# Optimization experiments

Measured on AMD Instinct MI355X. Metric: run time of the kernel, lower is better.

Reference implementation:

```python
import jax, jax.numpy as jnp
import numpy as np

N, E, H, IN, ED = 10000, 160000, 8, 128, 32
C1, C2 = 128, 128  # per-head channels of conv1 and conv2_1


def gat_conv(x, edge_index, edge_attr, W, We, att_s, att_d, att_e, bias, concat):
    """PyG GATConv with edge_dim, add_self_loops=True (fill_value='mean'), eval mode."""
    n = x.shape[0]
    h, c = att_s.shape
    src, dst = edge_index[0], edge_index[1]
    # self-loop edge_attr = per-node mean of incoming edge attrs (PyG fill_value='mean')
    deg = jax.ops.segment_sum(jnp.ones((src.shape[0],), x.dtype), dst, num_segments=n)
    loop_attr = jax.ops.segment_sum(edge_attr, dst, num_segments=n) / jnp.maximum(deg, 1.0)[:, None]
    loop = jnp.arange(n)
    src = jnp.concatenate([src, loop])
    dst = jnp.concatenate([dst, loop])
    ea = jnp.concatenate([edge_attr, loop_attr], axis=0)  # [E+N, ED]

    xh = (x @ W).reshape(n, h, c)                  # [N,H,C]
    a_s = jnp.sum(xh * att_s, axis=-1)             # [N,H]
    a_d = jnp.sum(xh * att_d, axis=-1)             # [N,H]
    eh = (ea @ We).reshape(-1, h, c)               # [E+N,H,C]
    a_e = jnp.sum(eh * att_e, axis=-1)             # [E+N,H]

    alpha = jax.nn.leaky_relu(a_s[src] + a_d[dst] + a_e, negative_slope=0.2)
    # segment softmax over incoming edges of each dst node (every node has a self loop)
    amax = jax.ops.segment_max(alpha, dst, num_segments=n)
    ex = jnp.exp(alpha - amax[dst])
    denom = jax.ops.segment_sum(ex, dst, num_segments=n)
    alpha = ex / (denom[dst] + 1e-16)

    out = jax.ops.segment_sum(xh[src] * alpha[:, :, None], dst, num_segments=n)  # [N,H,C]
    out = out.reshape(n, h * c) if concat else out.mean(axis=1)
    return out + bias


def setup_inputs() -> dict:
    key = jax.random.key(0)
    ks = jax.random.split(key, 16)
    s = 0.05
    return {
        "x": jax.random.normal(ks[0], (N, IN), jnp.float32),
        "edge_index": jax.random.randint(ks[1], (2, E), 0, N, dtype=jnp.int64),
        "edge_attr": jax.random.normal(ks[2], (E, ED), jnp.float32),
        # conv1: IN -> H*C1, concat=True
        "W1": jax.random.normal(ks[3], (IN, H * C1), jnp.float32) * s,
        "We1": jax.random.normal(ks[4], (ED, H * C1), jnp.float32) * s,
        "as1": jax.random.normal(ks[5], (H, C1), jnp.float32) * s,
        "ad1": jax.random.normal(ks[6], (H, C1), jnp.float32) * s,
        "ae1": jax.random.normal(ks[7], (H, C1), jnp.float32) * s,
        "b1": jnp.zeros((H * C1,), jnp.float32),
        # conv2_1: H*C1 -> C2, concat=False (Drugbank branch)
        "W2": jax.random.normal(ks[8], (H * C1, H * C2), jnp.float32) * s,
        "We2": jax.random.normal(ks[9], (ED, H * C2), jnp.float32) * s,
        "as2": jax.random.normal(ks[10], (H, C2), jnp.float32) * s,
        "ad2": jax.random.normal(ks[11], (H, C2), jnp.float32) * s,
        "ae2": jax.random.normal(ks[12], (H, C2), jnp.float32) * s,
        "b2": jnp.zeros((C2,), jnp.float32),
    }


def reference(x, edge_index, edge_attr, W1, We1, as1, ad1, ae1, b1,
              W2, We2, as2, ad2, ae2, b2):
    # dataset == 'Drugbank' path; dropout is identity in eval mode
    h = gat_conv(x, edge_index, edge_attr, W1, We1, as1, ad1, ae1, b1, concat=True)
    h = jax.nn.relu(h)
    out = gat_conv(h, edge_index, edge_attr, W2, We2, as2, ad2, ae2, b2, concat=False)
    return out
```

## Files before the change

kernel.cpp:

```cpp
#include <hip/hip_runtime.h>
#include <hip/hip_bf16.h>
#include <cstdint>
#include <cstddef>


#define EDD 32

typedef __attribute__((ext_vector_type(4))) float f32x4;
typedef __attribute__((ext_vector_type(8))) short bf16x8;
typedef __attribute__((ext_vector_type(8))) unsigned short u16x8;

__device__ inline unsigned short f2bf_rn(float f) {
  uint32_t u = __float_as_uint(f);
  return (unsigned short)((u + 0x7FFFu + ((u >> 16) & 1u)) >> 16);
}

__device__ inline float bf2f(unsigned short b) {
  return __uint_as_float(((uint32_t)b) << 16);
}

__device__ inline void gload_lds16(const void* g, void* l) {
  __builtin_amdgcn_global_load_lds((const __attribute__((address_space(1))) void*)g,
                                   (__attribute__((address_space(3))) void*)l, 16, 0, 0);
}


__global__ void deg_count_kernel(const int* __restrict__ ei, int* __restrict__ deg, int E) {
  int e = blockIdx.x * 256 + threadIdx.x;
  if (e < E) atomicAdd(&deg[ei[E + e]], 1);
}

__global__ void scan_kernel(const int* __restrict__ deg, int* __restrict__ rowptr,
                            int* __restrict__ cursor, int n) {
  __shared__ int wsum[16];
  int t = threadIdx.x;
  int chunk = (n + 1023) >> 10;
  int lo = min(t * chunk, n), hi = min(lo + chunk, n);
  int s = 0;
  for (int i = lo; i < hi; ++i) s += deg[i];
  int lane = t & 63, w = t >> 6;
  int v = s;
#pragma unroll
  for (int off = 1; off < 64; off <<= 1) {
    int u = __shfl_up(v, off);
    if (lane >= off) v += u;
  }
  if (lane == 63) wsum[w] = v;
  __syncthreads();
  if (t == 0) {
    int acc = 0;
#pragma unroll
    for (int i = 0; i < 16; ++i) { int x = wsum[i]; wsum[i] = acc; acc += x; }
  }
  __syncthreads();
  int excl = v - s + wsum[w];
  for (int i = lo; i < hi; ++i) {
    rowptr[i] = excl; cursor[i] = excl; excl += deg[i];
  }
  if (t == 1023) rowptr[n] = excl;
}

__global__ void scatter_kernel(const int* __restrict__ ei, int* __restrict__ cursor,
                               int* __restrict__ csr_src, int* __restrict__ csr_dst,
                               int* __restrict__ csr_eid, int E) {
  int e = blockIdx.x * 256 + threadIdx.x;
  if (e >= E) return;
  int d = ei[E + e];
  int pos = atomicAdd(&cursor[d], 1);
  csr_src[pos] = ei[e];
  csr_dst[pos] = d;
  csr_eid[pos] = e;
}

__global__ void permute_ea_kernel(const int* __restrict__ csr_eid,
                                  const float* __restrict__ edge_attr,
                                  float* __restrict__ ea_csr, int E) {
  int gid = blockIdx.x * 256 + threadIdx.x;
  if (gid >= E * 8) return;
  int p = gid >> 3, q = gid & 7;
  int e = csr_eid[p];
  ((float4*)ea_csr)[(size_t)p * 8 + q] = ((const float4*)edge_attr)[(size_t)e * 8 + q];
}

__global__ void loop_attr_kernel(const int* __restrict__ rowptr,
                                 const float* __restrict__ ea_csr,
                                 float* __restrict__ loop_attr, int N) {
  int n = blockIdx.x * 8 + (threadIdx.x >> 5);
  int lane = threadIdx.x & 31;
  if (n >= N) return;
  int r0 = rowptr[n], r1 = rowptr[n + 1];
  float s = 0.f;
  for (int p = r0; p < r1; ++p)
    s += ea_csr[(size_t)p * EDD + lane];
  float dv = fmaxf((float)(r1 - r0), 1.f);
  loop_attr[(size_t)n * EDD + lane] = s / dv;
}


__global__ void cvt_bf16_kernel(const float* __restrict__ in,
                                unsigned short* __restrict__ out, int n4) {
  int i = blockIdx.x * 256 + threadIdx.x;
  if (i >= n4) return;
  float4 v = ((const float4*)in)[i];
  ushort4 o;
  o.x = f2bf_rn(v.x); o.y = f2bf_rn(v.y); o.z = f2bf_rn(v.z); o.w = f2bf_rn(v.w);
  ((ushort4*)out)[i] = o;
}

__global__ void transpose_both_kernel(const float* __restrict__ W1, unsigned short* __restrict__ Bt1,
                                      const float* __restrict__ W2, unsigned short* __restrict__ Bt2) {
  __shared__ float tile[32][33];
  int by = blockIdx.y;
  const float* W; unsigned short* Bt; int K, bk;
  if (by < 4) { W = W1; Bt = Bt1; K = 128; bk = by * 32; }
  else        { W = W2; Bt = Bt2; K = 1024; bk = (by - 4) * 32; }
  int bn = blockIdx.x * 32;
  int tx = threadIdx.x & 31, ty = threadIdx.x >> 5;
  for (int r = ty; r < 32; r += 8)
    tile[r][tx] = W[(size_t)(bk + r) * 1024 + bn + tx];
  __syncthreads();
  for (int r = ty; r < 32; r += 8)
    Bt[(size_t)(bn + r) * K + bk + tx] = f2bf_rn(tile[tx][r]);
}

__global__ void ve_both_kernel(const float* __restrict__ We1, const float* __restrict__ ae1,
                               const float* __restrict__ We2, const float* __restrict__ ae2,
                               float* __restrict__ Ve) {
  int b = blockIdx.x;
  const float* We = b ? We2 : We1;
  const float* ae = b ? ae2 : ae1;
  int t = threadIdx.x;
  int d = t >> 3, h = t & 7;
  float s = 0.f;
  for (int c = 0; c < 128; ++c) s = fmaf(We[d * 1024 + h * 128 + c], ae[h * 128 + c], s);
  Ve[b * 256 + t] = s;
}


__global__ __launch_bounds__(256) void gemm1_fullk_kernel(
    const unsigned short* __restrict__ Abf, const unsigned short* __restrict__ Btbf,
    unsigned short* __restrict__ Cbf, float* __restrict__ a_s, float* __restrict__ a_d,
    const float* __restrict__ att_s, const float* __restrict__ att_d, int M) {
  __shared__ __align__(16) unsigned short lds[4 * 8192];
  __shared__ float redS[128][2];
  __shared__ float redD[128][2];
  const int t = threadIdx.x;
  const int lane = t & 63;
  const int wid = t >> 6;
  const int wr = wid >> 1, wc = wid & 1;
  const int m0 = blockIdx.y * 128;
  const int n0 = blockIdx.x * 128;
  const int hb = blockIdx.x;
  const int srow = lane >> 2;
  const int sg = lane & 3;

#pragma unroll
  for (int s = 0; s < 4; ++s) {
    unsigned short* L = lds + s * 8192;
    int k0 = s * 32;
#pragma unroll
    for (int q = 0; q < 2; ++q) {
      int rb = wid * 32 + q * 16;
      int row = rb + srow;
      int gsrc = sg ^ ((row >> 1) & 3);
      size_t ga = (size_t)(m0 + row) * 128 + k0 + gsrc * 8;
      size_t gb = (size_t)(n0 + row) * 128 + k0 + gsrc * 8;
      gload_lds16(Abf + ga, L + rb * 32);
      gload_lds16(Btbf + gb, L + 4096 + rb * 32);
    }
  }
  __syncthreads();

  int offa[4], offb[4];
#pragma unroll
  for (int i = 0; i < 4; ++i) {
    int rowa = wr * 64 + i * 16 + (lane & 15);
    offa[i] = rowa * 32 + (((lane >> 4) ^ ((rowa >> 1) & 3)) * 8);
    int rowb = wc * 64 + i * 16 + (lane & 15);
    offb[i] = rowb * 32 + (((lane >> 4) ^ ((rowb >> 1) & 3)) * 8);
  }

  f32x4 acc[4][4] = {};
#pragma unroll
  for (int s = 0; s < 4; ++s) {
    unsigned short* L = lds + s * 8192;
    bf16x8 ah[4];
#pragma unroll
    for (int i = 0; i < 4; ++i) ah[i] = *(const bf16x8*)(L + offa[i]);
#pragma unroll
    for (int j = 0; j < 4; ++j) {
      bf16x8 bh = *(const bf16x8*)(L + 4096 + offb[j]);
#pragma unroll
      for (int i = 0; i < 4; ++i)
        acc[i][j] = __builtin_amdgcn_mfma_f32_16x16x32_bf16(ah[i], bh, acc[i][j], 0, 0, 0);
    }
  }

  float as_v[4], ad_v[4];
#pragma unroll
  for (int j = 0; j < 4; ++j) {
    int c = n0 + wc * 64 + j * 16 + (lane & 15);
    as_v[j] = att_s[c];
    ad_v[j] = att_d[c];
  }
#pragma unroll
  for (int i = 0; i < 4; ++i) {
#pragma unroll
    for (int r = 0; r < 4; ++r) {
      float sA = 0.f, sD = 0.f;
#pragma unroll
      for (int j = 0; j < 4; ++j) {
        sA = fmaf(acc[i][j][r], as_v[j], sA);
        sD = fmaf(acc[i][j][r], ad_v[j], sD);
      }
#pragma unroll
      for (int mask = 1; mask <= 8; mask <<= 1) {
        sA += __shfl_xor(sA, mask);
        sD += __shfl_xor(sD, mask);
      }
      if ((lane & 15) == 0) {
        int ml = wr * 64 + i * 16 + (lane >> 4) * 4 + r;
        redS[ml][wc] = sA;
        redD[ml][wc] = sD;
      }
      int m = m0 + wr * 64 + i * 16 + (lane >> 4) * 4 + r;
      if (m < M) {
#pragma unroll
        for (int j = 0; j < 4; ++j) {
          int n = n0 + wc * 64 + j * 16 + (lane & 15);
          Cbf[(size_t)m * 1024 + n] = f2bf_rn(acc[i][j][r]);
        }
      }
    }
  }
  __syncthreads();
  if (t < 128) {
    int m = m0 + t;
    if (m < M) {
      a_s[(size_t)m * 8 + hb] = redS[t][0] + redS[t][1];
      a_d[(size_t)m * 8 + hb] = redD[t][0] + redD[t][1];
    }
  }
}


__global__ __launch_bounds__(256) void gemm2_dbuf_kernel(
    const unsigned short* __restrict__ Abf, const unsigned short* __restrict__ Btbf,
    unsigned short* __restrict__ Cbf, float* __restrict__ a_s, float* __restrict__ a_d,
    const float* __restrict__ att_s, const float* __restrict__ att_d, int M, int K) {
  __shared__ __align__(16) unsigned short lds[2 * 8192];
  __shared__ float redS[128][2];
  __shared__ float redD[128][2];
  const int t = threadIdx.x;
  const int lane = t & 63;
  const int wid = t >> 6;
  const int wr = wid >> 1, wc = wid & 1;
  const int m0 = blockIdx.y * 128;
  const int n0 = blockIdx.x * 128;
  const int hb = blockIdx.x;
  const int srow = lane >> 2;
  const int sg = lane & 3;
  const int nk = K >> 5;

  auto stage = [&](int b, int k) {
    unsigned short* L = lds + b * 8192;
    int k0 = k * 32;
#pragma unroll
    for (int q = 0; q < 2; ++q) {
      int rb = wid * 32 + q * 16;
      int row = rb + srow;
      int gsrc = sg ^ ((row >> 1) & 3);
      size_t ga = (size_t)(m0 + row) * K + k0 + gsrc * 8;
      size_t gb = (size_t)(n0 + row) * K + k0 + gsrc * 8;
      gload_lds16(Abf + ga, L + rb * 32);
      gload_lds16(Btbf + gb, L + 4096 + rb * 32);
    }
  };

  int offa[4], offb[4];
#pragma unroll
  for (int i = 0; i < 4; ++i) {
    int rowa = wr * 64 + i * 16 + (lane & 15);
    offa[i] = rowa * 32 + (((lane >> 4) ^ ((rowa >> 1) & 3)) * 8);
    int rowb = wc * 64 + i * 16 + (lane & 15);
    offb[i] = rowb * 32 + (((lane >> 4) ^ ((rowb >> 1) & 3)) * 8);
  }

  f32x4 acc[4][4] = {};
  stage(0, 0);
  __syncthreads();

  for (int k = 0; k < nk; ++k) {
    if (k + 1 < nk) stage((k + 1) & 1, k + 1);
    unsigned short* L = lds + (k & 1) * 8192;
    bf16x8 ah[4], bh[4];
#pragma unroll
    for (int i = 0; i < 4; ++i) ah[i] = *(const bf16x8*)(L + offa[i]);
#pragma unroll
    for (int j = 0; j < 4; ++j) bh[j] = *(const bf16x8*)(L + 4096 + offb[j]);
#pragma unroll
    for (int j = 0; j < 4; ++j)
#pragma unroll
      for (int i = 0; i < 4; ++i)
        acc[i][j] = __builtin_amdgcn_mfma_f32_16x16x32_bf16(ah[i], bh[j], acc[i][j], 0, 0, 0);
    __syncthreads();
  }

  float as_v[4], ad_v[4];
#pragma unroll
  for (int j = 0; j < 4; ++j) {
    int c = n0 + wc * 64 + j * 16 + (lane & 15);
    as_v[j] = att_s[c];
    ad_v[j] = att_d[c];
  }
#pragma unroll
  for (int i = 0; i < 4; ++i) {
#pragma unroll
    for (int r = 0; r < 4; ++r) {
      float sA = 0.f, sD = 0.f;
#pragma unroll
      for (int j = 0; j < 4; ++j) {
        sA = fmaf(acc[i][j][r], as_v[j], sA);
        sD = fmaf(acc[i][j][r], ad_v[j], sD);
      }
#pragma unroll
      for (int mask = 1; mask <= 8; mask <<= 1) {
        sA += __shfl_xor(sA, mask);
        sD += __shfl_xor(sD, mask);
      }
      if ((lane & 15) == 0) {
        int ml = wr * 64 + i * 16 + (lane >> 4) * 4 + r;
        redS[ml][wc] = sA;
        redD[ml][wc] = sD;
      }
      int m = m0 + wr * 64 + i * 16 + (lane >> 4) * 4 + r;
      if (m < M) {
#pragma unroll
        for (int j = 0; j < 4; ++j) {
          int n = n0 + wc * 64 + j * 16 + (lane & 15);
          Cbf[(size_t)m * 1024 + n] = f2bf_rn(acc[i][j][r]);
        }
      }
    }
  }
  __syncthreads();
  if (t < 128) {
    int m = m0 + t;
    if (m < M) {
      a_s[(size_t)m * 8 + hb] = redS[t][0] + redS[t][1];
      a_d[(size_t)m * 8 + hb] = redD[t][0] + redD[t][1];
    }
  }
}


__global__ __launch_bounds__(256) void edge_alpha_t_kernel(
    const int* __restrict__ csr_src, const int* __restrict__ csr_dst,
    const float* __restrict__ ea_csr, const float* __restrict__ loop_attr,
    const float* __restrict__ a_s, const float* __restrict__ a_d,
    const float* __restrict__ Ve,
    float* __restrict__ alpha_t, float* __restrict__ self_t, int E, int n) {
  __shared__ float sVe[EDD][8];
  int t = threadIdx.x;
  sVe[t >> 3][t & 7] = Ve[t];
  __syncthreads();
  int idx = blockIdx.x * 256 + t;
  if (idx >= E + n) return;
  int s, d;
  const float* ea;
  if (idx < E) {
    s = csr_src[idx]; d = csr_dst[idx];
    ea = ea_csr + (size_t)idx * EDD;
  } else {
    s = d = idx - E;
    ea = loop_attr + (size_t)(idx - E) * EDD;
  }
  float ae[8] = {0.f, 0.f, 0.f, 0.f, 0.f, 0.f, 0.f, 0.f};
#pragma unroll
  for (int k = 0; k < EDD; k += 4) {
    float4 v = *(const float4*)&ea[k];
#pragma unroll
    for (int h = 0; h < 8; ++h) {
      ae[h] = fmaf(v.x, sVe[k][h], ae[h]);
      ae[h] = fmaf(v.y, sVe[k + 1][h], ae[h]);
      ae[h] = fmaf(v.z, sVe[k + 2][h], ae[h]);
      ae[h] = fmaf(v.w, sVe[k + 3][h], ae[h]);
    }
  }
#pragma unroll
  for (int h = 0; h < 8; ++h) {
    float a = a_s[(size_t)s * 8 + h] + a_d[(size_t)d * 8 + h] + ae[h];
    a = (a > 0.f) ? a : 0.2f * a;
    if (idx < E) alpha_t[(size_t)h * E + idx] = a;
    else         self_t[(size_t)h * n + (idx - E)] = a;
  }
}


__global__ __launch_bounds__(256) void sm_weights_t_kernel(
    float* __restrict__ alpha_t, float* __restrict__ self_t,
    const int* __restrict__ rowptr, int N, int E) {
  int n = blockIdx.x * 4 + (threadIdx.x >> 6);
  int lane = threadIdx.x & 63;
  if (n >= N) return;
  int r0 = rowptr[n], deg = rowptr[n + 1] - r0;
  int h = lane >> 3, slot = lane & 7;
  float* pa = alpha_t + (size_t)h * E + r0;
  float m = -1e30f, s = 0.f;
  for (int i = slot; i < deg; i += 8) {
    float a = pa[i];
    if (a <= m) {
      s += __expf(a - m);
    } else {
      s = s * __expf(m - a) + 1.f;
      m = a;
    }
  }
#pragma unroll
  for (int mask = 1; mask <= 4; mask <<= 1) {
    float mo = __shfl_xor(m, mask);
    float so = __shfl_xor(s, mask);
    float mn = fmaxf(m, mo);
    s = s * __expf(m - mn) + so * __expf(mo - mn);
    m = mn;
  }
  float aself = self_t[(size_t)h * N + n];
  float mn = fmaxf(m, aself);
  s = s * __expf(m - mn) + __expf(aself - mn);
  float inv = 1.f / (s + 1e-16f);
  if (slot == 0) self_t[(size_t)h * N + n] = __expf(aself - mn) * inv;
  for (int i = slot; i < deg; i += 8)
    pa[i] = __expf(pa[i] - mn) * inv;
}


template <int RELU_BIAS>
__global__ __launch_bounds__(256) void agg_gather_h_kernel(
    const unsigned short* __restrict__ xbf, const float* __restrict__ alpha_t,
    const float* __restrict__ self_t, const int* __restrict__ rowptr,
    const int* __restrict__ csr_src, const float* __restrict__ bias,
    unsigned short* __restrict__ obf, int N, int E) {
  const int h = blockIdx.x & 7;
  const int g = blockIdx.x >> 3;
  const int t = threadIdx.x;
  const int n = g * 16 + (t >> 4);
  const int sub = t & 15;
  if (n >= N) return;
  const int r0 = rowptr[n], r1 = rowptr[n + 1];
  const float* __restrict__ pw = alpha_t + (size_t)h * E;
  const size_t cb = (size_t)h * 128 + sub * 8;
  float acc[8];
  {
    float ws = self_t[(size_t)h * N + n];
    u16x8 v = *(const u16x8*)(xbf + (size_t)n * 1024 + cb);
#pragma unroll
    for (int k = 0; k < 8; ++k) acc[k] = ws * bf2f(v[k]);
  }
  int p = r0;
  for (; p + 2 <= r1; p += 2) {
    float w0 = pw[p], w1 = pw[p + 1];
    int s0 = csr_src[p], s1 = csr_src[p + 1];
    u16x8 v0 = *(const u16x8*)(xbf + (size_t)s0 * 1024 + cb);
    u16x8 v1 = *(const u16x8*)(xbf + (size_t)s1 * 1024 + cb);
#pragma unroll
    for (int k = 0; k < 8; ++k) acc[k] = fmaf(w0, bf2f(v0[k]), acc[k]);
#pragma unroll
    for (int k = 0; k < 8; ++k) acc[k] = fmaf(w1, bf2f(v1[k]), acc[k]);
  }
  if (p < r1) {
    float w0 = pw[p];
    int s0 = csr_src[p];
    u16x8 v0 = *(const u16x8*)(xbf + (size_t)s0 * 1024 + cb);
#pragma unroll
    for (int k = 0; k < 8; ++k) acc[k] = fmaf(w0, bf2f(v0[k]), acc[k]);
  }
  u16x8 o;
  if (RELU_BIAS) {
    float4 b0 = *(const float4*)(bias + cb);
    float4 b1v = *(const float4*)(bias + cb + 4);
    float bb[8] = {b0.x, b0.y, b0.z, b0.w, b1v.x, b1v.y, b1v.z, b1v.w};
#pragma unroll
    for (int k = 0; k < 8; ++k) o[k] = f2bf_rn(fmaxf(acc[k] + bb[k], 0.f));
  } else {
#pragma unroll
    for (int k = 0; k < 8; ++k) o[k] = f2bf_rn(acc[k]);
  }
  *(u16x8*)(obf + (size_t)n * 1024 + cb) = o;
}


__global__ void head_reduce_kernel(const unsigned short* __restrict__ xpart,
                                   const float* __restrict__ b2,
                                   float* __restrict__ outp, int N) {
  int gid = blockIdx.x * 256 + threadIdx.x;
  if (gid >= N * 32) return;
  int n = gid >> 5, q = gid & 31;
  float sx = 0.f, sy = 0.f, sz = 0.f, sw = 0.f;
#pragma unroll
  for (int h = 0; h < 8; ++h) {
    ushort4 v = *(const ushort4*)(xpart + (size_t)n * 1024 + h * 128 + q * 4);
    sx += bf2f(v.x); sy += bf2f(v.y); sz += bf2f(v.z); sw += bf2f(v.w);
  }
  float4 b = ((const float4*)b2)[q];
  float4 o;
  o.x = sx * 0.125f + b.x;
  o.y = sy * 0.125f + b.y;
  o.z = sz * 0.125f + b.z;
  o.w = sw * 0.125f + b.w;
  ((float4*)outp)[(size_t)n * 32 + q] = o;
}


extern "C" void kernel_launch(void* const* d_in, const int* in_sizes, int n_in,
                              void* d_out, int out_size, void* d_ws, size_t ws_size,
                              hipStream_t stream) {
  const float* x        = (const float*)d_in[0];
  const int*   ei       = (const int*)d_in[1];
  const float* edge_attr= (const float*)d_in[2];
  const float* W1       = (const float*)d_in[3];
  const float* We1      = (const float*)d_in[4];
  const float* as1      = (const float*)d_in[5];
  const float* ad1      = (const float*)d_in[6];
  const float* ae1      = (const float*)d_in[7];
  const float* b1       = (const float*)d_in[8];
  const float* W2       = (const float*)d_in[9];
  const float* We2      = (const float*)d_in[10];
  const float* as2      = (const float*)d_in[11];
  const float* ad2      = (const float*)d_in[12];
  const float* ae2      = (const float*)d_in[13];
  const float* b2       = (const float*)d_in[14];
  float* out = (float*)d_out;

  const int N = in_sizes[0] / 128;
  const int E = in_sizes[2] / EDD;
  const int Mpad = ((N + 127) / 128) * 128;

  char* ws = (char*)d_ws;
  size_t off = 0;
  auto alloc = [&](size_t bytes) -> void* {
    void* p = ws + off;
    off = (off + bytes + 255) & ~(size_t)255;
    return p;
  };
  int*   deg       = (int*)alloc((size_t)N * 4);
  int*   rowptr    = (int*)alloc((size_t)(N + 1) * 4);
  int*   cursor    = (int*)alloc((size_t)N * 4);
  int*   csr_src   = (int*)alloc((size_t)E * 4);
  int*   csr_dst   = (int*)alloc((size_t)E * 4);
  int*   csr_eid   = (int*)alloc((size_t)E * 4);
  float* ea_csr    = (float*)alloc((size_t)E * EDD * 4);
  float* loop_attr = (float*)alloc((size_t)N * EDD * 4);
  float* a_s       = (float*)alloc((size_t)N * 8 * 4);
  float* a_d       = (float*)alloc((size_t)N * 8 * 4);
  float* Ve        = (float*)alloc(512 * 4);
  float* alpha_t   = (float*)alloc((size_t)E * 8 * 4);
  float* self_t    = (float*)alloc((size_t)N * 8 * 4);
  unsigned short* xh1bf = (unsigned short*)alloc((size_t)N * 1024 * 2);
  unsigned short* xh2bf = (unsigned short*)alloc((size_t)N * 1024 * 2);
  unsigned short* xpart = (unsigned short*)alloc((size_t)N * 1024 * 2);
  unsigned short* xbf   = (unsigned short*)alloc((size_t)Mpad * 128 * 2);
  unsigned short* Bt1   = (unsigned short*)alloc((size_t)1024 * 128 * 2);
  unsigned short* Bt2   = (unsigned short*)alloc((size_t)1024 * 1024 * 2);
  unsigned short* h1bf  = (unsigned short*)alloc((size_t)Mpad * 1024 * 2);
  (void)ws_size; (void)n_in; (void)out_size;

  hipMemsetAsync(deg, 0, (size_t)N * 4, stream);

  int gE = (E + 255) / 256;
  deg_count_kernel<<<gE, 256, 0, stream>>>(ei, deg, E);
  scan_kernel<<<1, 1024, 0, stream>>>(deg, rowptr, cursor, N);
  scatter_kernel<<<gE, 256, 0, stream>>>(ei, cursor, csr_src, csr_dst, csr_eid, E);
  permute_ea_kernel<<<(E * 8 + 255) / 256, 256, 0, stream>>>(csr_eid, edge_attr, ea_csr, E);
  loop_attr_kernel<<<(N + 7) / 8, 256, 0, stream>>>(rowptr, ea_csr, loop_attr, N);

  cvt_bf16_kernel<<<(N * 128 / 4 + 255) / 256, 256, 0, stream>>>(x, xbf, N * 128 / 4);
  transpose_both_kernel<<<dim3(32, 36), 256, 0, stream>>>(W1, Bt1, W2, Bt2);
  ve_both_kernel<<<2, 256, 0, stream>>>(We1, ae1, We2, ae2, Ve);

  dim3 ggrid(8, Mpad / 128);
  int gEA = (E + N + 255) / 256;
  int gSM = (N + 3) / 4;
  int gAG = 8 * ((N + 15) / 16);

  gemm1_fullk_kernel<<<ggrid, 256, 0, stream>>>(xbf, Bt1, xh1bf, a_s, a_d, as1, ad1, N);
  edge_alpha_t_kernel<<<gEA, 256, 0, stream>>>(csr_src, csr_dst, ea_csr, loop_attr,
                                               a_s, a_d, Ve, alpha_t, self_t, E, N);
  sm_weights_t_kernel<<<gSM, 256, 0, stream>>>(alpha_t, self_t, rowptr, N, E);
  agg_gather_h_kernel<1><<<gAG, 256, 0, stream>>>(xh1bf, alpha_t, self_t, rowptr, csr_src,
                                                  b1, h1bf, N, E);

  gemm2_dbuf_kernel<<<ggrid, 256, 0, stream>>>(h1bf, Bt2, xh2bf, a_s, a_d, as2, ad2, N, 1024);
  edge_alpha_t_kernel<<<gEA, 256, 0, stream>>>(csr_src, csr_dst, ea_csr, loop_attr,
                                               a_s, a_d, Ve + 256, alpha_t, self_t, E, N);
  sm_weights_t_kernel<<<gSM, 256, 0, stream>>>(alpha_t, self_t, rowptr, N, E);
  agg_gather_h_kernel<0><<<gAG, 256, 0, stream>>>(xh2bf, alpha_t, self_t, rowptr, csr_src,
                                                  nullptr, xpart, N, E);
  head_reduce_kernel<<<(N * 32 + 255) / 256, 256, 0, stream>>>(xpart, b2, out, N);
}
```

Before: 248.0 us.

## Fuse edge alpha with segment softmax, derive self-loop attr inline, register-load B

The separate per-edge alpha kernel and softmax kernel are merged into one per-node kernel. It computes edge logits, tracks an online max/sum, and gets the self-loop logit from the mean of edge logits, which holds because that logit is linear in edge_attr. This removes the loop_attr kernel, the csr_dst array and one round trip of alpha through memory. Separately, the second GEMM now loads B fragments straight from global memory into registers with prefetch, which halves LDS use but adds uncoalesced global loads and register pressure.

```diff
diff --git a/kernel.cpp b/kernel.cpp
--- a/kernel.cpp
+++ b/kernel.cpp
@@ -61,14 +61,12 @@
 }
 
 __global__ void scatter_kernel(const int* __restrict__ ei, int* __restrict__ cursor,
-                               int* __restrict__ csr_src, int* __restrict__ csr_dst,
-                               int* __restrict__ csr_eid, int E) {
+                               int* __restrict__ csr_src, int* __restrict__ csr_eid, int E) {
   int e = blockIdx.x * 256 + threadIdx.x;
   if (e >= E) return;
   int d = ei[E + e];
   int pos = atomicAdd(&cursor[d], 1);
   csr_src[pos] = ei[e];
-  csr_dst[pos] = d;
   csr_eid[pos] = e;
 }
 
@@ -80,20 +78,6 @@
   int p = gid >> 3, q = gid & 7;
   int e = csr_eid[p];
   ((float4*)ea_csr)[(size_t)p * 8 + q] = ((const float4*)edge_attr)[(size_t)e * 8 + q];
-}
-
-__global__ void loop_attr_kernel(const int* __restrict__ rowptr,
-                                 const float* __restrict__ ea_csr,
-                                 float* __restrict__ loop_attr, int N) {
-  int n = blockIdx.x * 8 + (threadIdx.x >> 5);
-  int lane = threadIdx.x & 31;
-  if (n >= N) return;
-  int r0 = rowptr[n], r1 = rowptr[n + 1];
-  float s = 0.f;
-  for (int p = r0; p < r1; ++p)
-    s += ea_csr[(size_t)p * EDD + lane];
-  float dv = fmaxf((float)(r1 - r0), 1.f);
-  loop_attr[(size_t)n * EDD + lane] = s / dv;
 }
 
 
@@ -244,11 +228,11 @@
 }
 
 
-__global__ __launch_bounds__(256) void gemm2_dbuf_kernel(
+__global__ __launch_bounds__(256) void gemm2_breg_kernel(
     const unsigned short* __restrict__ Abf, const unsigned short* __restrict__ Btbf,
     unsigned short* __restrict__ Cbf, float* __restrict__ a_s, float* __restrict__ a_d,
     const float* __restrict__ att_s, const float* __restrict__ att_d, int M, int K) {
-  __shared__ __align__(16) unsigned short lds[2 * 8192];
+  __shared__ __align__(16) unsigned short lds[2 * 4096];
   __shared__ float redS[128][2];
   __shared__ float redD[128][2];
   const int t = threadIdx.x;
@@ -262,8 +246,8 @@
   const int sg = lane & 3;
   const int nk = K >> 5;
 
-  auto stage = [&](int b, int k) {
-    unsigned short* L = lds + b * 8192;
+  auto stageA = [&](int b, int k) {
+    unsigned short* L = lds + b * 4096;
     int k0 = k * 32;
 #pragma unroll
     for (int q = 0; q < 2; ++q) {
@@ -271,38 +255,48 @@
       int row = rb + srow;
       int gsrc = sg ^ ((row >> 1) & 3);
       size_t ga = (size_t)(m0 + row) * K + k0 + gsrc * 8;
-      size_t gb = (size_t)(n0 + row) * K + k0 + gsrc * 8;
       gload_lds16(Abf + ga, L + rb * 32);
-      gload_lds16(Btbf + gb, L + 4096 + rb * 32);
     }
   };
 
-  int offa[4], offb[4];
+  const unsigned short* bbase = Btbf + (size_t)(n0 + wc * 64 + (lane & 15)) * K + (lane >> 4) * 8;
+  auto loadB = [&](bf16x8* b, int k0) {
+#pragma unroll
+    for (int j = 0; j < 4; ++j)
+      b[j] = *(const bf16x8*)(bbase + (size_t)j * 16 * K + k0);
+  };
+
+  int offa[4];
 #pragma unroll
   for (int i = 0; i < 4; ++i) {
     int rowa = wr * 64 + i * 16 + (lane & 15);
     offa[i] = rowa * 32 + (((lane >> 4) ^ ((rowa >> 1) & 3)) * 8);
-    int rowb = wc * 64 + i * 16 + (lane & 15);
-    offb[i] = rowb * 32 + (((lane >> 4) ^ ((rowb >> 1) & 3)) * 8);
   }
 
   f32x4 acc[4][4] = {};
-  stage(0, 0);
+  bf16x8 bcur[4], bnext[4];
+  stageA(0, 0);
+  loadB(bcur, 0);
   __syncthreads();
 
   for (int k = 0; k < nk; ++k) {
-    if (k + 1 < nk) stage((k + 1) & 1, k + 1);
-    unsigned short* L = lds + (k & 1) * 8192;
-    bf16x8 ah[4], bh[4];
+    if (k + 1 < nk) {
+      stageA((k + 1) & 1, k + 1);
+      loadB(bnext, (k + 1) * 32);
+    }
+    unsigned short* L = lds + (k & 1) * 4096;
+    bf16x8 ah[4];
 #pragma unroll
     for (int i = 0; i < 4; ++i) ah[i] = *(const bf16x8*)(L + offa[i]);
 #pragma unroll
-    for (int j = 0; j < 4; ++j) bh[j] = *(const bf16x8*)(L + 4096 + offb[j]);
-#pragma unroll
     for (int j = 0; j < 4; ++j)
 #pragma unroll
       for (int i = 0; i < 4; ++i)
-        acc[i][j] = __builtin_amdgcn_mfma_f32_16x16x32_bf16(ah[i], bh[j], acc[i][j], 0, 0, 0);
+        acc[i][j] = __builtin_amdgcn_mfma_f32_16x16x32_bf16(ah[i], bcur[j], acc[i][j], 0, 0, 0);
+    if (k + 1 < nk) {
+#pragma unroll
+      for (int j = 0; j < 4; ++j) bcur[j] = bnext[j];
+    }
     __syncthreads();
   }
 
@@ -354,61 +348,40 @@
 }
 
 
-__global__ __launch_bounds__(256) void edge_alpha_t_kernel(
-    const int* __restrict__ csr_src, const int* __restrict__ csr_dst,
-    const float* __restrict__ ea_csr, const float* __restrict__ loop_attr,
+__global__ __launch_bounds__(256) void alpha_sm_kernel(
+    const int* __restrict__ rowptr, const int* __restrict__ csr_src,
+    const float* __restrict__ ea_csr,
     const float* __restrict__ a_s, const float* __restrict__ a_d,
     const float* __restrict__ Ve,
-    float* __restrict__ alpha_t, float* __restrict__ self_t, int E, int n) {
+    float* __restrict__ alpha_t, float* __restrict__ self_t, int N, int E) {
   __shared__ float sVe[EDD][8];
   int t = threadIdx.x;
   sVe[t >> 3][t & 7] = Ve[t];
   __syncthreads();
-  int idx = blockIdx.x * 256 + t;
-  if (idx >= E + n) return;
-  int s, d;
-  const float* ea;
-  if (idx < E) {
-    s = csr_src[idx]; d = csr_dst[idx];
-    ea = ea_csr + (size_t)idx * EDD;
-  } else {
-    s = d = idx - E;
-    ea = loop_attr + (size_t)(idx - E) * EDD;
-  }
-  float ae[8] = {0.f, 0.f, 0.f, 0.f, 0.f, 0.f, 0.f, 0.f};
-#pragma unroll
-  for (int k = 0; k < EDD; k += 4) {
-    float4 v = *(const float4*)&ea[k];
-#pragma unroll
-    for (int h = 0; h < 8; ++h) {
-      ae[h] = fmaf(v.x, sVe[k][h], ae[h]);
-      ae[h] = fmaf(v.y, sVe[k + 1][h], ae[h]);
-      ae[h] = fmaf(v.z, sVe[k + 2][h], ae[h]);
-      ae[h] = fmaf(v.w, sVe[k + 3][h], ae[h]);
-    }
-  }
-#pragma unroll
-  for (int h = 0; h < 8; ++h) {
-    float a = a_s[(size_t)s * 8 + h] + a_d[(size_t)d * 8 + h] + ae[h];
+  int n = blockIdx.x * 4 + (t >> 6);
+  if (n >= N) return;
+  int lane = t & 63;
+  int e8 = lane >> 3, h = lane & 7;
+  int r0 = rowptr[n], deg = rowptr[n + 1] - r0;
+  float adn = a_d[(size_t)n * 8 + h];
+  float m = -1e30f, s = 0.f, aesum = 0.f;
+  for (int i = e8; i < deg; i += 8) {
+    int p = r0 + i;
+    int src = csr_src[p];
+    const float4* ea4 = (const float4*)(ea_csr + (size_t)p * EDD);
+    float ae = 0.f;
+#pragma unroll
+    for (int k = 0; k < 8; ++k) {
+      float4 v = ea4[k];
+      ae = fmaf(v.x, sVe[k * 4 + 0][h], ae);
+      ae = fmaf(v.y, sVe[k * 4 + 1][h], ae);
+      ae = fmaf(v.z, sVe[k * 4 + 2][h], ae);
+      ae = fmaf(v.w, sVe[k * 4 + 3][h], ae);
+    }
+    aesum += ae;
+    float a = a_s[(size_t)src * 8 + h] + adn + ae;
     a = (a > 0.f) ? a : 0.2f * a;
-    if (idx < E) alpha_t[(size_t)h * E + idx] = a;
-    else         self_t[(size_t)h * n + (idx - E)] = a;
-  }
-}
-
-
-__global__ __launch_bounds__(256) void sm_weights_t_kernel(
-    float* __restrict__ alpha_t, float* __restrict__ self_t,
-    const int* __restrict__ rowptr, int N, int E) {
-  int n = blockIdx.x * 4 + (threadIdx.x >> 6);
-  int lane = threadIdx.x & 63;
-  if (n >= N) return;
-  int r0 = rowptr[n], deg = rowptr[n + 1] - r0;
-  int h = lane >> 3, slot = lane & 7;
-  float* pa = alpha_t + (size_t)h * E + r0;
-  float m = -1e30f, s = 0.f;
-  for (int i = slot; i < deg; i += 8) {
-    float a = pa[i];
+    alpha_t[(size_t)h * E + p] = a;
     if (a <= m) {
       s += __expf(a - m);
     } else {
@@ -417,20 +390,25 @@
     }
   }
 #pragma unroll
-  for (int mask = 1; mask <= 4; mask <<= 1) {
+  for (int mask = 8; mask <= 32; mask <<= 1) {
     float mo = __shfl_xor(m, mask);
     float so = __shfl_xor(s, mask);
+    aesum += __shfl_xor(aesum, mask);
     float mn = fmaxf(m, mo);
     s = s * __expf(m - mn) + so * __expf(mo - mn);
     m = mn;
   }
-  float aself = self_t[(size_t)h * N + n];
+  float aeself = aesum / fmaxf((float)deg, 1.f);
+  float aself = a_s[(size_t)n * 8 + h] + adn + aeself;
+  aself = (aself > 0.f) ? aself : 0.2f * aself;
   float mn = fmaxf(m, aself);
   s = s * __expf(m - mn) + __expf(aself - mn);
   float inv = 1.f / (s + 1e-16f);
-  if (slot == 0) self_t[(size_t)h * N + n] = __expf(aself - mn) * inv;
-  for (int i = slot; i < deg; i += 8)
-    pa[i] = __expf(pa[i] - mn) * inv;
+  if (e8 == 0) self_t[(size_t)h * N + n] = __expf(aself - mn) * inv;
+  for (int i = e8; i < deg; i += 8) {
+    size_t p = (size_t)h * E + r0 + i;
+    alpha_t[p] = __expf(alpha_t[p] - mn) * inv;
+  }
 }
 
 
@@ -546,10 +524,8 @@
   int*   rowptr    = (int*)alloc((size_t)(N + 1) * 4);
   int*   cursor    = (int*)alloc((size_t)N * 4);
   int*   csr_src   = (int*)alloc((size_t)E * 4);
-  int*   csr_dst   = (int*)alloc((size_t)E * 4);
   int*   csr_eid   = (int*)alloc((size_t)E * 4);
   float* ea_csr    = (float*)alloc((size_t)E * EDD * 4);
-  float* loop_attr = (float*)alloc((size_t)N * EDD * 4);
   float* a_s       = (float*)alloc((size_t)N * 8 * 4);
   float* a_d       = (float*)alloc((size_t)N * 8 * 4);
   float* Ve        = (float*)alloc(512 * 4);
@@ -569,30 +545,26 @@
   int gE = (E + 255) / 256;
   deg_count_kernel<<<gE, 256, 0, stream>>>(ei, deg, E);
   scan_kernel<<<1, 1024, 0, stream>>>(deg, rowptr, cursor, N);
-  scatter_kernel<<<gE, 256, 0, stream>>>(ei, cursor, csr_src, csr_dst, csr_eid, E);
+  scatter_kernel<<<gE, 256, 0, stream>>>(ei, cursor, csr_src, csr_eid, E);
   permute_ea_kernel<<<(E * 8 + 255) / 256, 256, 0, stream>>>(csr_eid, edge_attr, ea_csr, E);
-  loop_attr_kernel<<<(N + 7) / 8, 256, 0, stream>>>(rowptr, ea_csr, loop_attr, N);
 
   cvt_bf16_kernel<<<(N * 128 / 4 + 255) / 256, 256, 0, stream>>>(x, xbf, N * 128 / 4);
   transpose_both_kernel<<<dim3(32, 36), 256, 0, stream>>>(W1, Bt1, W2, Bt2);
   ve_both_kernel<<<2, 256, 0, stream>>>(We1, ae1, We2, ae2, Ve);
 
   dim3 ggrid(8, Mpad / 128);
-  int gEA = (E + N + 255) / 256;
   int gSM = (N + 3) / 4;
   int gAG = 8 * ((N + 15) / 16);
 
   gemm1_fullk_kernel<<<ggrid, 256, 0, stream>>>(xbf, Bt1, xh1bf, a_s, a_d, as1, ad1, N);
-  edge_alpha_t_kernel<<<gEA, 256, 0, stream>>>(csr_src, csr_dst, ea_csr, loop_attr,
-                                               a_s, a_d, Ve, alpha_t, self_t, E, N);
-  sm_weights_t_kernel<<<gSM, 256, 0, stream>>>(alpha_t, self_t, rowptr, N, E);
+  alpha_sm_kernel<<<gSM, 256, 0, stream>>>(rowptr, csr_src, ea_csr, a_s, a_d, Ve,
+                                           alpha_t, self_t, N, E);
   agg_gather_h_kernel<1><<<gAG, 256, 0, stream>>>(xh1bf, alpha_t, self_t, rowptr, csr_src,
                                                   b1, h1bf, N, E);
 
-  gemm2_dbuf_kernel<<<ggrid, 256, 0, stream>>>(h1bf, Bt2, xh2bf, a_s, a_d, as2, ad2, N, 1024);
-  edge_alpha_t_kernel<<<gEA, 256, 0, stream>>>(csr_src, csr_dst, ea_csr, loop_attr,
-                                               a_s, a_d, Ve + 256, alpha_t, self_t, E, N);
-  sm_weights_t_kernel<<<gSM, 256, 0, stream>>>(alpha_t, self_t, rowptr, N, E);
+  gemm2_breg_kernel<<<ggrid, 256, 0, stream>>>(h1bf, Bt2, xh2bf, a_s, a_d, as2, ad2, N, 1024);
+  alpha_sm_kernel<<<gSM, 256, 0, stream>>>(rowptr, csr_src, ea_csr, a_s, a_d, Ve + 256,
+                                           alpha_t, self_t, N, E);
   agg_gather_h_kernel<0><<<gAG, 256, 0, stream>>>(xh2bf, alpha_t, self_t, rowptr, csr_src,
                                                   nullptr, xpart, N, E);
   head_reduce_kernel<<<(N * 32 + 255) / 256, 256, 0, stream>>>(xpart, b2, out, N);
```

Result: slower. 255.9 us (+3.2%).
